# Kernel tuning notes

Hardware: AMD Instinct MI355X
Metric: run time of the kernel (lower is better)

Reference implementation:

```python
import jax, jax.numpy as jnp
import numpy as np

N_NODES = 50000
N_EDGES = 400000
F_IN = 70
E_DIM = 4
HID = 128
HEADS = 4


def _add_self_loops(src, dst, edge_attr, n):
    # PyG GATConv(add_self_loops=True, fill_value='mean' when edge_dim is set):
    # self-loop edge_attr = per-dst-node mean of incoming edge_attr.
    cnt = jax.ops.segment_sum(jnp.ones((src.shape[0],), edge_attr.dtype), dst, n)
    loop_attr = jax.ops.segment_sum(edge_attr, dst, n) / jnp.clip(cnt, 1.0)[:, None]
    loop = jnp.arange(n, dtype=src.dtype)
    return (jnp.concatenate([src, loop]), jnp.concatenate([dst, loop]),
            jnp.concatenate([edge_attr, loop_attr], axis=0))


def _gat_layer(x, src, dst, e_attr, W, a_src, a_dst, We, a_edge, b, concat):
    # W: [in, H*D]; a_src/a_dst/a_edge: [H, D]; We: [edge_dim, H*D]
    n = x.shape[0]
    H, D = a_src.shape
    xs = (x @ W).reshape(n, H, D)                      # [N,H,D]
    s_src = jnp.einsum('nhd,hd->nh', xs, a_src)        # [N,H]
    s_dst = jnp.einsum('nhd,hd->nh', xs, a_dst)
    ee = (e_attr @ We).reshape(-1, H, D)               # [E,H,D]
    s_edge = jnp.einsum('ehd,hd->eh', ee, a_edge)
    alpha = jax.nn.leaky_relu(s_src[src] + s_dst[dst] + s_edge, 0.2)  # [E,H]
    # segment softmax over edges grouped by destination node
    m = jax.ops.segment_max(alpha, dst, n)
    m = jnp.where(jnp.isfinite(m), m, 0.0)
    ex = jnp.exp(alpha - m[dst])
    denom = jax.ops.segment_sum(ex, dst, n)
    alpha = ex / (denom[dst] + 1e-16)
    msg = xs[src] * alpha[..., None]                   # [E,H,D] -- dominant traffic
    agg = jax.ops.segment_sum(msg, dst, n)             # [N,H,D]
    out = agg.reshape(n, H * D) if concat else agg.mean(axis=1)
    return out + b


def _layer_norm(x, g, b, eps=1e-5):
    mu = x.mean(-1, keepdims=True)
    var = ((x - mu) ** 2).mean(-1, keepdims=True)
    return (x - mu) * jax.lax.rsqrt(var + eps) * g + b


def setup_inputs() -> dict:
    key = jax.random.key(0)
    ks = jax.random.split(key, 24)
    f32 = jnp.float32
    node_features = jax.random.normal(ks[0], (N_NODES, F_IN), f32)
    edge_index = jax.random.randint(ks[1], (2, N_EDGES), 0, N_NODES, jnp.int32)
    edge_attr = jax.random.uniform(ks[2], (N_EDGES, E_DIM), f32)
    s = 0.1
    return {
        'node_features': node_features,
        'edge_index': edge_index,
        'edge_attr': edge_attr,
        'W1': jax.random.normal(ks[3], (F_IN, HEADS * HID), f32) * s,
        'as1': jax.random.normal(ks[4], (HEADS, HID), f32) * s,
        'ad1': jax.random.normal(ks[5], (HEADS, HID), f32) * s,
        'We1': jax.random.normal(ks[6], (E_DIM, HEADS * HID), f32) * s,
        'ae1': jax.random.normal(ks[7], (HEADS, HID), f32) * s,
        'b1': jnp.zeros((HEADS * HID,), f32),
        # GAT layer 2: 512 -> 128, 1 head, mean
        'W2': jax.random.normal(ks[8], (HEADS * HID, HID), f32) * s,
        'as2': jax.random.normal(ks[9], (1, HID), f32) * s,
        'ad2': jax.random.normal(ks[10], (1, HID), f32) * s,
        'We2': jax.random.normal(ks[11], (E_DIM, HID), f32) * s,
        'ae2': jax.random.normal(ks[12], (1, HID), f32) * s,
        'b2': jnp.zeros((HID,), f32),
        'ln_g': jnp.ones((HID,), f32),
        'ln_b': jnp.zeros((HID,), f32),
        'pw': jax.random.normal(ks[13], (HID, 8), f32) * s,
        'pb': jnp.zeros((8,), f32),
        'dw': jax.random.normal(ks[14], (HID, 4), f32) * s,
        'db': jnp.zeros((4,), f32),
    }


def reference(node_features, edge_index, edge_attr, W1, as1, ad1, We1, ae1, b1,
              W2, as2, ad2, We2, ae2, b2, ln_g, ln_b, pw, pb, dw, db):
    n = node_features.shape[0]
    src, dst, ea = _add_self_loops(edge_index[0], edge_index[1], edge_attr, n)
    x = jax.nn.gelu(_gat_layer(node_features, src, dst, ea, W1, as1, ad1, We1, ae1, b1, True), approximate=False)
    x = jax.nn.gelu(_gat_layer(x, src, dst, ea, W2, as2, ad2, We2, ae2, b2, False), approximate=False)
    x = _layer_norm(x, ln_g, ln_b)
    return (x @ pw + pb, x @ dw + db)
```

## Files before the change

kernel.cpp:

```cpp
#include <hip/hip_runtime.h>
#include <hip/hip_bf16.h>
#include <math.h>

#define NN 50000
#define NE 400000
#define FIN 70
#define EDIM 4
#define HIDD 128
#define NHEAD 4
constexpr int ET = NE + NN;
constexpr int KP1 = 96;
constexpr int NFP = 72;
constexpr int SCB = (NN + 255) / 256;

constexpr size_t al4(size_t x){ return (x + 3) & ~size_t(3); }
constexpr size_t CNT_O   = 0;
constexpr size_t ZEND    = al4(CNT_O + NN);
constexpr size_t CSR_O   = ZEND;
constexpr size_t BSUM_O  = al4(CSR_O + NN + 1);
constexpr size_t BOFF_O  = al4(BSUM_O + 256);
constexpr size_t EPK_O   = al4(BOFF_O + 256);
constexpr size_t EXF1_O  = al4(EPK_O + (size_t)ET*4);
constexpr size_t EXF2_O  = al4(EXF1_O + (size_t)ET*4);
constexpr size_t SS1_O   = al4(EXF2_O + ET);
constexpr size_t SD1_O   = al4(SS1_O + (size_t)NN*4);
constexpr size_t SS2_O   = al4(SD1_O + (size_t)NN*4);
constexpr size_t SD2_O   = al4(SS2_O + NN);
constexpr size_t CST_O   = al4(SD2_O + NN);
constexpr size_t W1T_O   = al4(CST_O + 2048);
constexpr size_t W2T_O   = al4(W1T_O + 4*128*KP1/2);
constexpr size_t NFB_O   = al4(W2T_O + 128*512/2);
constexpr size_t AGG_O   = al4(NFB_O + (size_t)NN*NFP/2);
constexpr size_t XS2_O   = al4(AGG_O + (size_t)4*NN*KP1/2);

constexpr int VS1 = 0;
constexpr int VD1 = 320;
constexpr int VE1 = 640;
constexpr int VE2 = 656;
constexpr int VS2 = 704;
constexpr int VD2 = 1216;

typedef short s8v __attribute__((ext_vector_type(8)));
typedef float f4v __attribute__((ext_vector_type(4)));

__device__ __forceinline__ unsigned short f2b(float v){
  __hip_bfloat16 b = __float2bfloat16(v);
  return *(unsigned short*)&b;
}
__device__ __forceinline__ float b2f(unsigned u_lo16){
  return __uint_as_float(u_lo16 << 16);
}
__device__ __forceinline__ unsigned pk2(float lo, float hi){
  return (unsigned)f2b(lo) | ((unsigned)f2b(hi) << 16);
}
__device__ __forceinline__ float lrelu(float x){ return x > 0.f ? x : 0.2f * x; }

__device__ __forceinline__ float gelu_fast(float x){
  float z = x * 0.70710678118654752440f;
  float a = fabsf(z);
  float t = 1.f / (1.f + 0.3275911f * a);
  float p = ((((1.061405429f*t - 1.453152027f)*t + 1.421413741f)*t
              - 0.284496736f)*t + 0.254829592f)*t;
  float erfv = 1.f - p * __expf(-a * a);
  erfv = copysignf(erfv, z);
  return 0.5f * x * (1.f + erfv);
}

__global__ void k_deg(const int* __restrict__ ei, int* __restrict__ cnt){
  int e = blockIdx.x * 256 + threadIdx.x;
  if (e >= NE) return;
  atomicAdd(&cnt[ei[NE + e]], 1);
}

__global__ void k_scan1(const int* __restrict__ cnt, int* __restrict__ bsum){
  __shared__ int ws[4];
  int t = threadIdx.x, lane = t & 63, w = t >> 6;
  int i = blockIdx.x * 256 + t;
  int v = (i < NN) ? cnt[i] + 1 : 0;
  for (int o = 32; o; o >>= 1) v += __shfl_down(v, o);
  if (lane == 0) ws[w] = v;
  __syncthreads();
  if (t == 0) bsum[blockIdx.x] = ws[0] + ws[1] + ws[2] + ws[3];
}

__global__ void k_scan2(const int* __restrict__ bsum, int* __restrict__ boff){
  __shared__ int ws[4];
  int t = threadIdx.x, lane = t & 63, w = t >> 6;
  int v = (t < SCB) ? bsum[t] : 0;
  int x = v;
  #pragma unroll
  for (int o = 1; o < 64; o <<= 1){ int u = __shfl_up(x, o); if (lane >= o) x += u; }
  if (lane == 63) ws[w] = x;
  __syncthreads();
  if (w == 0 && lane < 4){
    int y = ws[lane];
    #pragma unroll
    for (int o = 1; o < 4; o <<= 1){ int u = __shfl_up(y, o); if (lane >= o) y += u; }
    ws[lane] = y;
  }
  __syncthreads();
  int incl = x + (w > 0 ? ws[w - 1] : 0);
  if (t < SCB) boff[t] = incl - v;
}

__global__ void k_scan3(const int* __restrict__ cnt, const int* __restrict__ boff,
                        int* __restrict__ csr){
  __shared__ int ws[4];
  int t = threadIdx.x, lane = t & 63, w = t >> 6;
  int i = blockIdx.x * 256 + t;
  int v = (i < NN) ? cnt[i] + 1 : 0;
  int x = v;
  #pragma unroll
  for (int o = 1; o < 64; o <<= 1){ int u = __shfl_up(x, o); if (lane >= o) x += u; }
  if (lane == 63) ws[w] = x;
  __syncthreads();
  if (w == 0 && lane < 4){
    int y = ws[lane];
    #pragma unroll
    for (int o = 1; o < 4; o <<= 1){ int u = __shfl_up(y, o); if (lane >= o) y += u; }
    ws[lane] = y;
  }
  __syncthreads();
  if (i < NN) csr[i + 1] = boff[blockIdx.x] + (w > 0 ? ws[w - 1] : 0) + x;
  if (i == 0) csr[0] = 0;
}

__global__ void k_fill(const int* __restrict__ ei, const float* __restrict__ ea,
                       const int* __restrict__ csr, int* __restrict__ cnt,
                       int4* __restrict__ epk, const float* __restrict__ ss1,
                       const float* __restrict__ sd1, const float* __restrict__ C,
                       float4* __restrict__ exf){
  int e = blockIdx.x * 256 + threadIdx.x;
  if (e >= NE) return;
  int s = ei[e], d = ei[NE + e];
  int r = atomicSub(&cnt[d], 1);
  int p = csr[d] + r - 1;
  float4 a = *(const float4*)&ea[(size_t)e * 4];
  epk[p] = make_int4(s, d, (int)pk2(a.x, a.y), (int)pk2(a.z, a.w));
  float4 ssv = *(const float4*)&ss1[(size_t)s * 4];
  float4 sdv = *(const float4*)&sd1[(size_t)d * 4];
  float e0 = __expf(lrelu(ssv.x + sdv.x + a.x*C[VE1+0] + a.y*C[VE1+4] + a.z*C[VE1+8]  + a.w*C[VE1+12]));
  float e1 = __expf(lrelu(ssv.y + sdv.y + a.x*C[VE1+1] + a.y*C[VE1+5] + a.z*C[VE1+9]  + a.w*C[VE1+13]));
  float e2 = __expf(lrelu(ssv.z + sdv.z + a.x*C[VE1+2] + a.y*C[VE1+6] + a.z*C[VE1+10] + a.w*C[VE1+14]));
  float e3 = __expf(lrelu(ssv.w + sdv.w + a.x*C[VE1+3] + a.y*C[VE1+7] + a.z*C[VE1+11] + a.w*C[VE1+15]));
  exf[p] = make_float4(e0, e1, e2, e3);
}

__global__ void k_loopself(const int* __restrict__ csr, int4* __restrict__ epk,
                           const float* __restrict__ ss1, const float* __restrict__ sd1,
                           const float* __restrict__ C, float4* __restrict__ exf){
  int n = blockIdx.x * 256 + threadIdx.x;
  if (n >= NN) return;
  int a = csr[n], b = csr[n + 1];
  int deg = b - a - 1;
  float s0 = 0.f, s1 = 0.f, s2 = 0.f, s3 = 0.f;
  for (int p = a; p < b - 1; ++p){
    int4 v = epk[p];
    s0 += b2f((unsigned)v.z & 0xffffu); s1 += b2f((unsigned)v.z >> 16);
    s2 += b2f((unsigned)v.w & 0xffffu); s3 += b2f((unsigned)v.w >> 16);
  }
  float inv = 1.f / (float)(deg > 1 ? deg : 1);
  float m0 = s0*inv, m1 = s1*inv, m2 = s2*inv, m3 = s3*inv;
  epk[b - 1] = make_int4(n, n, (int)pk2(m0, m1), (int)pk2(m2, m3));
  float4 ssv = *(const float4*)&ss1[(size_t)n * 4];
  float4 sdv = *(const float4*)&sd1[(size_t)n * 4];
  float e0 = __expf(lrelu(ssv.x + sdv.x + m0*C[VE1+0] + m1*C[VE1+4] + m2*C[VE1+8]  + m3*C[VE1+12]));
  float e1 = __expf(lrelu(ssv.y + sdv.y + m0*C[VE1+1] + m1*C[VE1+5] + m2*C[VE1+9]  + m3*C[VE1+13]));
  float e2 = __expf(lrelu(ssv.z + sdv.z + m0*C[VE1+2] + m1*C[VE1+6] + m2*C[VE1+10] + m3*C[VE1+14]));
  float e3 = __expf(lrelu(ssv.w + sdv.w + m0*C[VE1+3] + m1*C[VE1+7] + m2*C[VE1+11] + m3*C[VE1+15]));
  exf[b - 1] = make_float4(e0, e1, e2, e3);
}

__global__ void k_prep(const float* __restrict__ W1, const float* __restrict__ as1,
                       const float* __restrict__ ad1, const float* __restrict__ We1,
                       const float* __restrict__ ae1, const float* __restrict__ W2,
                       const float* __restrict__ as2, const float* __restrict__ ad2,
                       const float* __restrict__ We2, const float* __restrict__ ae2,
                       float* __restrict__ C){
  int t = threadIdx.x;
  if (t < 280){
    int k = t >> 2, h = t & 3;
    float s = 0.f, d = 0.f;
    for (int dd = 0; dd < 128; ++dd){
      float w = W1[k*512 + h*128 + dd];
      s += w * as1[h*128 + dd];
      d += w * ad1[h*128 + dd];
    }
    C[VS1 + t] = s; C[VD1 + t] = d;
  }
  if (t < 16){
    int k = t >> 2, h = t & 3;
    float s = 0.f;
    for (int dd = 0; dd < 128; ++dd) s += We1[k*512 + h*128 + dd] * ae1[h*128 + dd];
    C[VE1 + t] = s;
  }
  if (t < 4){
    float s = 0.f;
    for (int dd = 0; dd < 128; ++dd) s += We2[t*128 + dd] * ae2[dd];
    C[VE2 + t] = s;
  }
  {
    float s = 0.f, d = 0.f;
    for (int dd = 0; dd < 128; ++dd){
      float w = W2[t*128 + dd];
      s += w * as2[dd];
      d += w * ad2[dd];
    }
    C[VS2 + t] = s; C[VD2 + t] = d;
  }
}

__global__ void k_tw(const float* __restrict__ W1, const float* __restrict__ W2,
                     unsigned short* __restrict__ W1t, unsigned short* __restrict__ W2t){
  int i = blockIdx.x * 256 + threadIdx.x;
  if (i < 4*128*KP1){
    int k = i % KP1, n = (i / KP1) & 127, h = i / (KP1*128);
    float v = (k < FIN) ? W1[k*512 + h*128 + n] : 0.f;
    W1t[i] = f2b(v);
  } else {
    int j = i - 4*128*KP1;
    if (j < 128*512){
      int k = j & 511, n = j >> 9;
      W2t[j] = f2b(W2[k*128 + n]);
    }
  }
}

__global__ __launch_bounds__(256) void k_cnfs1(const float* __restrict__ nf,
    const float* __restrict__ C, unsigned short* __restrict__ nfb,
    float* __restrict__ ss1, float* __restrict__ sd1){
  int lane = threadIdx.x & 63, w = threadIdx.x >> 6;
  int n = blockIdx.x * 4 + w;
  if (n >= NN) return;
  int c0 = lane * 2;
  bool act = lane < 35;
  float v0 = 0.f, v1 = 0.f;
  if (act){
    v0 = nf[(size_t)n * FIN + c0];
    v1 = nf[(size_t)n * FIN + c0 + 1];
  }
  if (lane < 36) *(unsigned*)&nfb[(size_t)n * NFP + c0] = act ? pk2(v0, v1) : 0u;
  float sh[4] = {0,0,0,0}, dh[4] = {0,0,0,0};
  if (act){
    float4 cs0 = *(const float4*)&C[VS1 + c0*4];
    float4 cs1 = *(const float4*)&C[VS1 + (c0+1)*4];
    float4 cd0 = *(const float4*)&C[VD1 + c0*4];
    float4 cd1 = *(const float4*)&C[VD1 + (c0+1)*4];
    sh[0] = v0*cs0.x + v1*cs1.x; sh[1] = v0*cs0.y + v1*cs1.y;
    sh[2] = v0*cs0.z + v1*cs1.z; sh[3] = v0*cs0.w + v1*cs1.w;
    dh[0] = v0*cd0.x + v1*cd1.x; dh[1] = v0*cd0.y + v1*cd1.y;
    dh[2] = v0*cd0.z + v1*cd1.z; dh[3] = v0*cd0.w + v1*cd1.w;
  }
  #pragma unroll
  for (int o = 32; o; o >>= 1){
    #pragma unroll
    for (int h = 0; h < 4; ++h){
      sh[h] += __shfl_xor(sh[h], o);
      dh[h] += __shfl_xor(dh[h], o);
    }
  }
  if (lane == 0){
    *(float4*)&ss1[(size_t)n*4] = make_float4(sh[0], sh[1], sh[2], sh[3]);
    *(float4*)&sd1[(size_t)n*4] = make_float4(dh[0], dh[1], dh[2], dh[3]);
  }
}

__global__ void k_al2(const int4* __restrict__ epk, const float* __restrict__ ss2,
                      const float* __restrict__ sd2, const float* __restrict__ C,
                      float* __restrict__ ex2){
  int p = blockIdx.x * 256 + threadIdx.x;
  if (p >= ET) return;
  int4 pk = epk[p];
  int s = pk.x, d = pk.y;
  float ax = b2f((unsigned)pk.z & 0xffffu), ay = b2f((unsigned)pk.z >> 16);
  float az = b2f((unsigned)pk.w & 0xffffu), aw = b2f((unsigned)pk.w >> 16);
  ex2[p] = __expf(lrelu(ss2[s] + sd2[d] +
             ax*C[VE2] + ay*C[VE2+1] + az*C[VE2+2] + aw*C[VE2+3]));
}

__global__ __launch_bounds__(256) void k_gemm12(
    const unsigned short* __restrict__ agg, const unsigned short* __restrict__ W1t,
    const unsigned short* __restrict__ W2t, const float* __restrict__ b1,
    const float* __restrict__ Cv, unsigned short* __restrict__ xs2b,
    float* __restrict__ ss2, float* __restrict__ sd2){
  __shared__ unsigned short xt[32 * 520];
  __shared__ unsigned short Bs[128 * 40];
  __shared__ unsigned short As[32 * 40];
  __shared__ float ssp[32][2], sdp[32][2];
  int tid = threadIdx.x, lane = tid & 63, w = tid >> 6;
  int wm = w & 1, wn = w >> 1;
  int m15 = lane & 15, rq = lane >> 4;
  int r0 = blockIdx.x * 32;
  int lrow = wm * 16 + m15;
  float s2a = 0.f, s2d = 0.f;
  constexpr size_t HS = (size_t)NN * KP1;
  for (int h = 0; h < 4; ++h){
    f4v acc[4] = {};
    const unsigned short* Ah = agg + (size_t)h * HS;
    const unsigned short* Wh = W1t + h * 128 * KP1;
    for (int k0 = 0; k0 < KP1; k0 += 32){
      if (tid < 128){
        int r = tid >> 2, c = tid & 3;
        int gr = r0 + r; if (gr >= NN) gr = NN - 1;
        *(uint4*)&As[r*40 + c*8] = *(const uint4*)&Ah[(size_t)gr*KP1 + k0 + c*8];
      }
      #pragma unroll
      for (int i = 0; i < 2; ++i){
        int idx = tid + i*256;
        int r = idx >> 2, c = idx & 3;
        *(uint4*)&Bs[r*40 + c*8] = *(const uint4*)&Wh[r*KP1 + k0 + c*8];
      }
      __syncthreads();
      s8v af = *(const s8v*)&As[lrow*40 + rq*8];
      #pragma unroll
      for (int ni = 0; ni < 4; ++ni){
        s8v bf = *(const s8v*)&Bs[(wn*64 + ni*16 + m15)*40 + rq*8];
        acc[ni] = __builtin_amdgcn_mfma_f32_16x16x32_bf16(bf, af, acc[ni], 0, 0, 0);
      }
      __syncthreads();
    }
    #pragma unroll
    for (int ni = 0; ni < 4; ++ni){
      int cb = h*128 + wn*64 + ni*16 + rq*4;
      float4 bv = *(const float4*)&b1[cb];
      float v0 = gelu_fast(acc[ni][0] + bv.x);
      float v1 = gelu_fast(acc[ni][1] + bv.y);
      float v2 = gelu_fast(acc[ni][2] + bv.z);
      float v3 = gelu_fast(acc[ni][3] + bv.w);
      float4 cs = *(const float4*)&Cv[VS2 + cb];
      float4 cd = *(const float4*)&Cv[VD2 + cb];
      s2a += v0*cs.x + v1*cs.y + v2*cs.z + v3*cs.w;
      s2d += v0*cd.x + v1*cd.y + v2*cd.z + v3*cd.w;
      *(uint2*)&xt[lrow*520 + cb] = make_uint2(pk2(v0,v1), pk2(v2,v3));
    }
  }
  s2a += __shfl_xor(s2a, 16); s2a += __shfl_xor(s2a, 32);
  s2d += __shfl_xor(s2d, 16); s2d += __shfl_xor(s2d, 32);
  if (rq == 0){ ssp[lrow][wn] = s2a; sdp[lrow][wn] = s2d; }
  __syncthreads();
  if (tid < 32 && r0 + tid < NN){
    ss2[r0 + tid] = ssp[tid][0] + ssp[tid][1];
    sd2[r0 + tid] = sdp[tid][0] + sdp[tid][1];
  }
  f4v acc2[4] = {};
  for (int k0 = 0; k0 < 512; k0 += 32){
    #pragma unroll
    for (int i = 0; i < 2; ++i){
      int idx = tid + i*256;
      int r = idx >> 2, c = idx & 3;
      *(uint4*)&Bs[r*40 + c*8] = *(const uint4*)&W2t[r*512 + k0 + c*8];
    }
    __syncthreads();
    s8v af = *(const s8v*)&xt[lrow*520 + k0 + rq*8];
    #pragma unroll
    for (int ni = 0; ni < 4; ++ni){
      s8v bf = *(const s8v*)&Bs[(wn*64 + ni*16 + m15)*40 + rq*8];
      acc2[ni] = __builtin_amdgcn_mfma_f32_16x16x32_bf16(bf, af, acc2[ni], 0, 0, 0);
    }
    __syncthreads();
  }
  int grow = r0 + lrow;
  if (grow < NN){
    #pragma unroll
    for (int ni = 0; ni < 4; ++ni){
      int gc = wn*64 + ni*16 + rq*4;
      *(uint2*)&xs2b[(size_t)grow*128 + gc] =
          make_uint2(pk2(acc2[ni][0], acc2[ni][1]), pk2(acc2[ni][2], acc2[ni][3]));
    }
  }
}

__global__ __launch_bounds__(256) void k_aggnf(const int* __restrict__ csr,
    const int4* __restrict__ epk, const float4* __restrict__ exf,
    const unsigned short* __restrict__ nfb, unsigned short* __restrict__ agg){
  int lane = threadIdx.x & 63, w = threadIdx.x >> 6;
  int n = blockIdx.x * 4 + w;
  if (n >= NN) return;
  int off = __builtin_amdgcn_readfirstlane(csr[n]);
  int end = __builtin_amdgcn_readfirstlane(csr[n + 1]);
  int col = lane * 2;
  bool act = lane < 36;
  float d0=0,d1=0,d2=0,d3=0;
  float a00=0,a01=0,a10=0,a11=0,a20=0,a21=0,a30=0,a31=0;
  int p = off;
  for (; p + 2 <= end; p += 2){
    int s0 = epk[p].x, s1 = epk[p+1].x;
    float4 e0 = exf[p], e1 = exf[p+1];
    unsigned u0 = 0, u1 = 0;
    if (act){
      u0 = *(const unsigned*)&nfb[(size_t)s0 * NFP + col];
      u1 = *(const unsigned*)&nfb[(size_t)s1 * NFP + col];
    }
    d0 += e0.x + e1.x; d1 += e0.y + e1.y; d2 += e0.z + e1.z; d3 += e0.w + e1.w;
    float v00 = b2f(u0 & 0xffffu), v01 = b2f(u0 >> 16);
    float v10 = b2f(u1 & 0xffffu), v11 = b2f(u1 >> 16);
    a00 += e0.x*v00 + e1.x*v10; a01 += e0.x*v01 + e1.x*v11;
    a10 += e0.y*v00 + e1.y*v10; a11 += e0.y*v01 + e1.y*v11;
    a20 += e0.z*v00 + e1.z*v10; a21 += e0.z*v01 + e1.z*v11;
    a30 += e0.w*v00 + e1.w*v10; a31 += e0.w*v01 + e1.w*v11;
  }
  if (p < end){
    int s0 = epk[p].x;
    float4 e0 = exf[p];
    unsigned u0 = 0;
    if (act) u0 = *(const unsigned*)&nfb[(size_t)s0 * NFP + col];
    d0 += e0.x; d1 += e0.y; d2 += e0.z; d3 += e0.w;
    float v00 = b2f(u0 & 0xffffu), v01 = b2f(u0 >> 16);
    a00 += e0.x*v00; a01 += e0.x*v01;
    a10 += e0.y*v00; a11 += e0.y*v01;
    a20 += e0.z*v00; a21 += e0.z*v01;
    a30 += e0.w*v00; a31 += e0.w*v01;
  }
  float i0 = 1.f/(d0+1e-16f), i1 = 1.f/(d1+1e-16f);
  float i2 = 1.f/(d2+1e-16f), i3 = 1.f/(d3+1e-16f);
  constexpr size_t HS = (size_t)NN * KP1;
  size_t base = (size_t)n * KP1 + col;
  if (act){
    *(unsigned*)&agg[base]        = pk2(a00*i0, a01*i0);
    *(unsigned*)&agg[base +   HS] = pk2(a10*i1, a11*i1);
    *(unsigned*)&agg[base + 2*HS] = pk2(a20*i2, a21*i2);
    *(unsigned*)&agg[base + 3*HS] = pk2(a30*i3, a31*i3);
  } else if (lane < 48){
    *(unsigned*)&agg[base]        = 0u;
    *(unsigned*)&agg[base +   HS] = 0u;
    *(unsigned*)&agg[base + 2*HS] = 0u;
    *(unsigned*)&agg[base + 3*HS] = 0u;
  }
}

__global__ __launch_bounds__(256) void k_agg2(
    const int* __restrict__ csr, const int4* __restrict__ epk,
    const float* __restrict__ ex2, const unsigned short* __restrict__ xs2b,
    const float* __restrict__ b2, const float* __restrict__ lng,
    const float* __restrict__ lnb, const float* __restrict__ pw,
    const float* __restrict__ pb, const float* __restrict__ dwm,
    const float* __restrict__ dbv, float* __restrict__ out){
  int lane = threadIdx.x & 63, w = threadIdx.x >> 6;
  int n = blockIdx.x * 4 + w;
  if (n >= NN) return;
  int off = __builtin_amdgcn_readfirstlane(csr[n]);
  int end = __builtin_amdgcn_readfirstlane(csr[n + 1]);
  int c0 = lane * 2;
  float acc0 = 0.f, acc1 = 0.f, den = 0.f;
  int p = off;
  for (; p + 4 <= end; p += 4){
    int s0 = epk[p].x, s1 = epk[p+1].x, s2 = epk[p+2].x, s3 = epk[p+3].x;
    float e0 = ex2[p], e1 = ex2[p+1], e2 = ex2[p+2], e3 = ex2[p+3];
    unsigned u0 = *(const unsigned*)&xs2b[(size_t)s0 * 128 + c0];
    unsigned u1 = *(const unsigned*)&xs2b[(size_t)s1 * 128 + c0];
    unsigned u2 = *(const unsigned*)&xs2b[(size_t)s2 * 128 + c0];
    unsigned u3 = *(const unsigned*)&xs2b[(size_t)s3 * 128 + c0];
    den += (e0 + e1) + (e2 + e3);
    acc0 += e0*b2f(u0 & 0xffffu) + e1*b2f(u1 & 0xffffu)
          + e2*b2f(u2 & 0xffffu) + e3*b2f(u3 & 0xffffu);
    acc1 += e0*b2f(u0 >> 16) + e1*b2f(u1 >> 16)
          + e2*b2f(u2 >> 16) + e3*b2f(u3 >> 16);
  }
  for (; p + 2 <= end; p += 2){
    int s0 = epk[p].x, s1 = epk[p+1].x;
    float e0 = ex2[p], e1 = ex2[p+1];
    unsigned u0 = *(const unsigned*)&xs2b[(size_t)s0 * 128 + c0];
    unsigned u1 = *(const unsigned*)&xs2b[(size_t)s1 * 128 + c0];
    den += e0 + e1;
    acc0 += e0*b2f(u0 & 0xffffu) + e1*b2f(u1 & 0xffffu);
    acc1 += e0*b2f(u0 >> 16) + e1*b2f(u1 >> 16);
  }
  if (p < end){
    int s0 = epk[p].x;
    float e0 = ex2[p];
    unsigned u0 = *(const unsigned*)&xs2b[(size_t)s0 * 128 + c0];
    den += e0;
    acc0 += e0*b2f(u0 & 0xffffu);
    acc1 += e0*b2f(u0 >> 16);
  }
  float invd = 1.f / (den + 1e-16f);
  float g0 = gelu_fast(acc0 * invd + b2[c0]);
  float g1 = gelu_fast(acc1 * invd + b2[c0 + 1]);
  float s = g0 + g1;
  #pragma unroll
  for (int o = 32; o; o >>= 1) s += __shfl_xor(s, o);
  float mu = s * (1.f / 128.f);
  float e0 = g0 - mu, e1 = g1 - mu;
  float q = e0*e0 + e1*e1;
  #pragma unroll
  for (int o = 32; o; o >>= 1) q += __shfl_xor(q, o);
  float rstd = rsqrtf(q * (1.f / 128.f) + 1e-5f);
  float y0 = e0 * rstd * lng[c0] + lnb[c0];
  float y1 = e1 * rstd * lng[c0 + 1] + lnb[c0 + 1];
  float pr[12];
  #pragma unroll
  for (int jj = 0; jj < 8; ++jj) pr[jj] = y0 * pw[c0*8 + jj] + y1 * pw[(c0+1)*8 + jj];
  #pragma unroll
  for (int jj = 0; jj < 4; ++jj) pr[8+jj] = y0 * dwm[c0*4 + jj] + y1 * dwm[(c0+1)*4 + jj];
  #pragma unroll
  for (int o = 32; o; o >>= 1)
    #pragma unroll
    for (int jj = 0; jj < 12; ++jj) pr[jj] += __shfl_xor(pr[jj], o);
  if (lane == 0){
    #pragma unroll
    for (int jj = 0; jj < 8; ++jj) out[(size_t)n*8 + jj] = pr[jj] + pb[jj];
    #pragma unroll
    for (int jj = 0; jj < 4; ++jj) out[(size_t)NN*8 + (size_t)n*4 + jj] = pr[8+jj] + dbv[jj];
  }
}

extern "C" void kernel_launch(void* const* d_in, const int* in_sizes, int n_in,
                              void* d_out, int out_size, void* d_ws, size_t ws_size,
                              hipStream_t stream){
  const float* nf  = (const float*)d_in[0];
  const int*   ei  = (const int*)  d_in[1];
  const float* ea  = (const float*)d_in[2];
  const float* W1  = (const float*)d_in[3];
  const float* as1 = (const float*)d_in[4];
  const float* ad1 = (const float*)d_in[5];
  const float* We1 = (const float*)d_in[6];
  const float* ae1 = (const float*)d_in[7];
  const float* b1  = (const float*)d_in[8];
  const float* W2  = (const float*)d_in[9];
  const float* as2 = (const float*)d_in[10];
  const float* ad2 = (const float*)d_in[11];
  const float* We2 = (const float*)d_in[12];
  const float* ae2 = (const float*)d_in[13];
  const float* b2  = (const float*)d_in[14];
  const float* lng = (const float*)d_in[15];
  const float* lnb = (const float*)d_in[16];
  const float* pw  = (const float*)d_in[17];
  const float* pb  = (const float*)d_in[18];
  const float* dw  = (const float*)d_in[19];
  const float* db  = (const float*)d_in[20];
  float* out = (float*)d_out;

  float* wf = (float*)d_ws;
  int*      cnt  = (int*)     (wf + CNT_O);
  int*      csr  = (int*)     (wf + CSR_O);
  int*      bsum = (int*)     (wf + BSUM_O);
  int*      boff = (int*)     (wf + BOFF_O);
  int4*     epk  = (int4*)    (wf + EPK_O);
  float4*   exf1 = (float4*)  (wf + EXF1_O);
  float*    ex2  =            (wf + EXF2_O);
  float*    ss1  =            (wf + SS1_O);
  float*    sd1  =            (wf + SD1_O);
  float*    ss2  =            (wf + SS2_O);
  float*    sd2  =            (wf + SD2_O);
  float*    Cc   =            (wf + CST_O);
  unsigned short* W1t = (unsigned short*)(wf + W1T_O);
  unsigned short* W2t = (unsigned short*)(wf + W2T_O);
  unsigned short* nfb = (unsigned short*)(wf + NFB_O);
  unsigned short* agg = (unsigned short*)(wf + AGG_O);
  unsigned short* xs2b= (unsigned short*)(wf + XS2_O);

  hipMemsetAsync(cnt, 0, NN * sizeof(int), stream);
  k_prep<<<1, 512, 0, stream>>>(W1, as1, ad1, We1, ae1, W2, as2, ad2, We2, ae2, Cc);
  k_tw<<<(4*128*KP1 + 128*512 + 255) / 256, 256, 0, stream>>>(W1, W2, W1t, W2t);
  k_cnfs1<<<(NN + 3) / 4, 256, 0, stream>>>(nf, Cc, nfb, ss1, sd1);
  k_deg<<<(NE + 255) / 256, 256, 0, stream>>>(ei, cnt);
  k_scan1<<<SCB, 256, 0, stream>>>(cnt, bsum);
  k_scan2<<<1, 256, 0, stream>>>(bsum, boff);
  k_scan3<<<SCB, 256, 0, stream>>>(cnt, boff, csr);
  k_fill<<<(NE + 255) / 256, 256, 0, stream>>>(ei, ea, csr, cnt, epk, ss1, sd1, Cc, exf1);
  k_loopself<<<(NN + 255) / 256, 256, 0, stream>>>(csr, epk, ss1, sd1, Cc, exf1);
  k_aggnf<<<(NN + 3) / 4, 256, 0, stream>>>(csr, epk, exf1, nfb, agg);
  k_gemm12<<<(NN + 31) / 32, 256, 0, stream>>>(agg, W1t, W2t, b1, Cc, xs2b, ss2, sd2);
  k_al2<<<(ET + 255) / 256, 256, 0, stream>>>(epk, ss2, sd2, Cc, ex2);
  k_agg2<<<(NN + 3) / 4, 256, 0, stream>>>(csr, epk, ex2, xs2b,
                                           b2, lng, lnb, pw, pb, dw, db, out);
}
```

Baseline: 364.2 us.

## Double-buffer and register-prefetch B tiles in fused GEMM kernel, load A directly

Restructures k_gemm12 so the weight tiles are prefetched into registers one step ahead and written into a double-buffered shared-memory array, removing one __syncthreads per k-step. The A operand (aggregated features) is now read straight from global memory into MFMA fragments, prefetched one head ahead, instead of being staged through shared memory. Shared padding changes from 40/520 to 36/516 and launch bounds request three blocks per CU. The aim is to overlap global loads with MFMA work and cut barrier stalls, at the cost of more registers and possible LDS bank conflicts from the new padding.

```diff
diff --git a/kernel.cpp b/kernel.cpp
--- a/kernel.cpp
+++ b/kernel.cpp
@@ -278,93 +278,124 @@
              ax*C[VE2] + ay*C[VE2+1] + az*C[VE2+2] + aw*C[VE2+3]));
 }
 
-__global__ __launch_bounds__(256) void k_gemm12(
+__global__ __launch_bounds__(256, 3) void k_gemm12(
     const unsigned short* __restrict__ agg, const unsigned short* __restrict__ W1t,
     const unsigned short* __restrict__ W2t, const float* __restrict__ b1,
     const float* __restrict__ Cv, unsigned short* __restrict__ xs2b,
     float* __restrict__ ss2, float* __restrict__ sd2){
-  __shared__ unsigned short xt[32 * 520];
-  __shared__ unsigned short Bs[128 * 40];
-  __shared__ unsigned short As[32 * 40];
+  __shared__ unsigned short xt[32 * 516];
+  __shared__ unsigned short Bs[2][128 * 36];
   __shared__ float ssp[32][2], sdp[32][2];
   int tid = threadIdx.x, lane = tid & 63, w = tid >> 6;
   int wm = w & 1, wn = w >> 1;
   int m15 = lane & 15, rq = lane >> 4;
   int r0 = blockIdx.x * 32;
   int lrow = wm * 16 + m15;
+  int gr = r0 + lrow; if (gr >= NN) gr = NN - 1;
   float s2a = 0.f, s2d = 0.f;
   constexpr size_t HS = (size_t)NN * KP1;
+
+  int br0 = tid >> 2, bc0 = tid & 3;
+  int br1 = br0 + 64;
+  int bw0 = br0 * 36 + bc0 * 8;
+  int bw1 = br1 * 36 + bc0 * 8;
+
+  uint4 breg0 = *(const uint4*)&W1t[br0 * KP1 + bc0 * 8];
+  uint4 breg1 = *(const uint4*)&W1t[br1 * KP1 + bc0 * 8];
+  s8v afc0, afc1, afc2, afn0, afn1, afn2;
+  {
+    const unsigned short* Ah = agg + (size_t)gr * KP1 + rq * 8;
+    afc0 = *(const s8v*)(Ah);
+    afc1 = *(const s8v*)(Ah + 32);
+    afc2 = *(const s8v*)(Ah + 64);
+  }
+
   for (int h = 0; h < 4; ++h){
     f4v acc[4] = {};
-    const unsigned short* Ah = agg + (size_t)h * HS;
-    const unsigned short* Wh = W1t + h * 128 * KP1;
-    for (int k0 = 0; k0 < KP1; k0 += 32){
-      if (tid < 128){
-        int r = tid >> 2, c = tid & 3;
-        int gr = r0 + r; if (gr >= NN) gr = NN - 1;
-        *(uint4*)&As[r*40 + c*8] = *(const uint4*)&Ah[(size_t)gr*KP1 + k0 + c*8];
+    #pragma unroll
+    for (int kf = 0; kf < 3; ++kf){
+      int buf = (h * 3 + kf) & 1;
+      unsigned short* Bb = Bs[buf];
+      *(uint4*)&Bb[bw0] = breg0;
+      *(uint4*)&Bb[bw1] = breg1;
+      __syncthreads();
+      if (kf == 0 && h < 3){
+        const unsigned short* Ah = agg + (size_t)(h + 1) * HS + (size_t)gr * KP1 + rq * 8;
+        afn0 = *(const s8v*)(Ah);
+        afn1 = *(const s8v*)(Ah + 32);
+        afn2 = *(const s8v*)(Ah + 64);
       }
-      #pragma unroll
-      for (int i = 0; i < 2; ++i){
-        int idx = tid + i*256;
-        int r = idx >> 2, c = idx & 3;
-        *(uint4*)&Bs[r*40 + c*8] = *(const uint4*)&Wh[r*KP1 + k0 + c*8];
+      if (kf < 2){
+        const unsigned short* Wn = W1t + h * (128 * KP1) + (kf + 1) * 32;
+        breg0 = *(const uint4*)&Wn[br0 * KP1 + bc0 * 8];
+        breg1 = *(const uint4*)&Wn[br1 * KP1 + bc0 * 8];
+      } else if (h < 3){
+        const unsigned short* Wn = W1t + (h + 1) * (128 * KP1);
+        breg0 = *(const uint4*)&Wn[br0 * KP1 + bc0 * 8];
+        breg1 = *(const uint4*)&Wn[br1 * KP1 + bc0 * 8];
+      } else {
+        breg0 = *(const uint4*)&W2t[br0 * 512 + bc0 * 8];
+        breg1 = *(const uint4*)&W2t[br1 * 512 + bc0 * 8];
       }
-      __syncthreads();
-      s8v af = *(const s8v*)&As[lrow*40 + rq*8];
+      s8v af = (kf == 0) ? afc0 : (kf == 1) ? afc1 : afc2;
       #pragma unroll
       for (int ni = 0; ni < 4; ++ni){
-        s8v bf = *(const s8v*)&Bs[(wn*64 + ni*16 + m15)*40 + rq*8];
+        s8v bf = *(const s8v*)&Bb[(wn * 64 + ni * 16 + m15) * 36 + rq * 8];
         acc[ni] = __builtin_amdgcn_mfma_f32_16x16x32_bf16(bf, af, acc[ni], 0, 0, 0);
       }
-      __syncthreads();
-    }
-    #pragma unroll
-    for (int ni = 0; ni < 4; ++ni){
-      int cb = h*128 + wn*64 + ni*16 + rq*4;
-      float4 bv = *(const float4*)&b1[cb];
-      float v0 = gelu_fast(acc[ni][0] + bv.x);
-      float v1 = gelu_fast(acc[ni][1] + bv.y);
-      float v2 = gelu_fast(acc[ni][2] + bv.z);
-      float v3 = gelu_fast(acc[ni][3] + bv.w);
-      float4 cs = *(const float4*)&Cv[VS2 + cb];
-      float4 cd = *(const float4*)&Cv[VD2 + cb];
-      s2a += v0*cs.x + v1*cs.y + v2*cs.z + v3*cs.w;
-      s2d += v0*cd.x + v1*cd.y + v2*cd.z + v3*cd.w;
-      *(uint2*)&xt[lrow*520 + cb] = make_uint2(pk2(v0,v1), pk2(v2,v3));
+      if (kf == 2){
+        #pragma unroll
+        for (int ni = 0; ni < 4; ++ni){
+          int cb = h * 128 + wn * 64 + ni * 16 + rq * 4;
+          float4 bv = *(const float4*)&b1[cb];
+          float v0 = gelu_fast(acc[ni][0] + bv.x);
+          float v1 = gelu_fast(acc[ni][1] + bv.y);
+          float v2 = gelu_fast(acc[ni][2] + bv.z);
+          float v3 = gelu_fast(acc[ni][3] + bv.w);
+          float4 cs = *(const float4*)&Cv[VS2 + cb];
+          float4 cd = *(const float4*)&Cv[VD2 + cb];
+          s2a += v0*cs.x + v1*cs.y + v2*cs.z + v3*cs.w;
+          s2d += v0*cd.x + v1*cd.y + v2*cd.z + v3*cd.w;
+          *(uint2*)&xt[lrow * 516 + cb] = make_uint2(pk2(v0, v1), pk2(v2, v3));
+        }
+        afc0 = afn0; afc1 = afn1; afc2 = afn2;
+      }
     }
   }
   s2a += __shfl_xor(s2a, 16); s2a += __shfl_xor(s2a, 32);
   s2d += __shfl_xor(s2d, 16); s2d += __shfl_xor(s2d, 32);
   if (rq == 0){ ssp[lrow][wn] = s2a; sdp[lrow][wn] = s2d; }
-  __syncthreads();
-  if (tid < 32 && r0 + tid < NN){
-    ss2[r0 + tid] = ssp[tid][0] + ssp[tid][1];
-    sd2[r0 + tid] = sdp[tid][0] + sdp[tid][1];
-  }
+
   f4v acc2[4] = {};
-  for (int k0 = 0; k0 < 512; k0 += 32){
-    #pragma unroll
-    for (int i = 0; i < 2; ++i){
-      int idx = tid + i*256;
-      int r = idx >> 2, c = idx & 3;
-      *(uint4*)&Bs[r*40 + c*8] = *(const uint4*)&W2t[r*512 + k0 + c*8];
-    }
+  #pragma unroll 2
+  for (int p = 0; p < 16; ++p){
+    int buf = p & 1;
+    unsigned short* Bb = Bs[buf];
+    *(uint4*)&Bb[bw0] = breg0;
+    *(uint4*)&Bb[bw1] = breg1;
     __syncthreads();
-    s8v af = *(const s8v*)&xt[lrow*520 + k0 + rq*8];
+    if (p == 0 && tid < 32 && r0 + tid < NN){
+      ss2[r0 + tid] = ssp[tid][0] + ssp[tid][1];
+      sd2[r0 + tid] = sdp[tid][0] + sdp[tid][1];
+    }
+    if (p < 15){
+      const unsigned short* Wn = W2t + (p + 1) * 32;
+      breg0 = *(const uint4*)&Wn[br0 * 512 + bc0 * 8];
+      breg1 = *(const uint4*)&Wn[br1 * 512 + bc0 * 8];
+    }
+    s8v af = *(const s8v*)&xt[lrow * 516 + p * 32 + rq * 8];
     #pragma unroll
     for (int ni = 0; ni < 4; ++ni){
-      s8v bf = *(const s8v*)&Bs[(wn*64 + ni*16 + m15)*40 + rq*8];
+      s8v bf = *(const s8v*)&Bb[(wn * 64 + ni * 16 + m15) * 36 + rq * 8];
       acc2[ni] = __builtin_amdgcn_mfma_f32_16x16x32_bf16(bf, af, acc2[ni], 0, 0, 0);
     }
-    __syncthreads();
   }
   int grow = r0 + lrow;
   if (grow < NN){
     #pragma unroll
     for (int ni = 0; ni < 4; ++ni){
-      int gc = wn*64 + ni*16 + rq*4;
-      *(uint2*)&xs2b[(size_t)grow*128 + gc] =
+      int gc = wn * 64 + ni * 16 + rq * 4;
+      *(uint2*)&xs2b[(size_t)grow * 128 + gc] =
           make_uint2(pk2(acc2[ni][0], acc2[ni][1]), pk2(acc2[ni][2], acc2[ni][3]));
     }
   }
```

After: 436.1 us. +19.7%, slower.

## Prepack weights into MFMA fragment layout and load operands directly from global

Applied to the files above, without the earlier changes.

Rewrites the weight transpose kernel to emit W1 and W2 in a per-k-chunk fragment-major layout, so each lane of k_gemm12 can load its MFMA B operand straight from global/L2. The shared-memory staging buffers and all the per-k-step __syncthreads in both GEMM phases are removed, and the A operand for layer 1 is also read directly from global. The xt row pitch changes to 516 and launch bounds request 4 blocks per CU to raise occupancy. This trades LDS staging and barriers for redundant global/L2 reads of the small weight matrices across waves.

```diff
diff --git a/kernel.cpp b/kernel.cpp
--- a/kernel.cpp
+++ b/kernel.cpp
@@ -211,17 +211,19 @@
 }
 
 __global__ void k_tw(const float* __restrict__ W1, const float* __restrict__ W2,
-                     unsigned short* __restrict__ W1t, unsigned short* __restrict__ W2t){
+                     unsigned short* __restrict__ W1p, unsigned short* __restrict__ W2p){
   int i = blockIdx.x * 256 + threadIdx.x;
-  if (i < 4*128*KP1){
-    int k = i % KP1, n = (i / KP1) & 127, h = i / (KP1*128);
-    float v = (k < FIN) ? W1[k*512 + h*128 + n] : 0.f;
-    W1t[i] = f2b(v);
+  if (i < 12*128*32){
+    int kk = i & 31, r = (i >> 5) & 127, ph = i >> 12;
+    int h = ph / 3, kf = ph - 3*h;
+    int kg = kf*32 + kk;
+    float v = (kg < FIN) ? W1[kg*512 + h*128 + r] : 0.f;
+    W1p[i] = f2b(v);
   } else {
-    int j = i - 4*128*KP1;
-    if (j < 128*512){
-      int k = j & 511, n = j >> 9;
-      W2t[j] = f2b(W2[k*128 + n]);
+    int j = i - 12*128*32;
+    if (j < 16*128*32){
+      int kk = j & 31, r = (j >> 5) & 127, p = j >> 12;
+      W2p[j] = f2b(W2[(p*32 + kk)*128 + r]);
     }
   }
 }
@@ -278,50 +280,39 @@
              ax*C[VE2] + ay*C[VE2+1] + az*C[VE2+2] + aw*C[VE2+3]));
 }
 
-__global__ __launch_bounds__(256) void k_gemm12(
-    const unsigned short* __restrict__ agg, const unsigned short* __restrict__ W1t,
-    const unsigned short* __restrict__ W2t, const float* __restrict__ b1,
+__global__ __launch_bounds__(256, 4) void k_gemm12(
+    const unsigned short* __restrict__ agg, const unsigned short* __restrict__ W1p,
+    const unsigned short* __restrict__ W2p, const float* __restrict__ b1,
     const float* __restrict__ Cv, unsigned short* __restrict__ xs2b,
     float* __restrict__ ss2, float* __restrict__ sd2){
-  __shared__ unsigned short xt[32 * 520];
-  __shared__ unsigned short Bs[128 * 40];
-  __shared__ unsigned short As[32 * 40];
+  __shared__ unsigned short xt[32 * 516];
   __shared__ float ssp[32][2], sdp[32][2];
   int tid = threadIdx.x, lane = tid & 63, w = tid >> 6;
   int wm = w & 1, wn = w >> 1;
   int m15 = lane & 15, rq = lane >> 4;
   int r0 = blockIdx.x * 32;
   int lrow = wm * 16 + m15;
+  int gr = r0 + lrow; if (gr >= NN) gr = NN - 1;
   float s2a = 0.f, s2d = 0.f;
   constexpr size_t HS = (size_t)NN * KP1;
+  const int bfo = (wn * 64 + m15) * 32 + rq * 8;
+
   for (int h = 0; h < 4; ++h){
     f4v acc[4] = {};
-    const unsigned short* Ah = agg + (size_t)h * HS;
-    const unsigned short* Wh = W1t + h * 128 * KP1;
-    for (int k0 = 0; k0 < KP1; k0 += 32){
-      if (tid < 128){
-        int r = tid >> 2, c = tid & 3;
-        int gr = r0 + r; if (gr >= NN) gr = NN - 1;
-        *(uint4*)&As[r*40 + c*8] = *(const uint4*)&Ah[(size_t)gr*KP1 + k0 + c*8];
-      }
-      #pragma unroll
-      for (int i = 0; i < 2; ++i){
-        int idx = tid + i*256;
-        int r = idx >> 2, c = idx & 3;
-        *(uint4*)&Bs[r*40 + c*8] = *(const uint4*)&Wh[r*KP1 + k0 + c*8];
-      }
-      __syncthreads();
-      s8v af = *(const s8v*)&As[lrow*40 + rq*8];
+    const unsigned short* Ah = agg + (size_t)h * HS + (size_t)gr * KP1 + rq * 8;
+    #pragma unroll
+    for (int kf = 0; kf < 3; ++kf){
+      s8v af = *(const s8v*)(Ah + kf * 32);
+      const unsigned short* Bp = W1p + (h * 3 + kf) * 4096 + bfo;
       #pragma unroll
       for (int ni = 0; ni < 4; ++ni){
-        s8v bf = *(const s8v*)&Bs[(wn*64 + ni*16 + m15)*40 + rq*8];
+        s8v bf = *(const s8v*)(Bp + ni * 512);
         acc[ni] = __builtin_amdgcn_mfma_f32_16x16x32_bf16(bf, af, acc[ni], 0, 0, 0);
       }
-      __syncthreads();
     }
     #pragma unroll
     for (int ni = 0; ni < 4; ++ni){
-      int cb = h*128 + wn*64 + ni*16 + rq*4;
+      int cb = h * 128 + wn * 64 + ni * 16 + rq * 4;
       float4 bv = *(const float4*)&b1[cb];
       float v0 = gelu_fast(acc[ni][0] + bv.x);
       float v1 = gelu_fast(acc[ni][1] + bv.y);
@@ -331,40 +322,37 @@
       float4 cd = *(const float4*)&Cv[VD2 + cb];
       s2a += v0*cs.x + v1*cs.y + v2*cs.z + v3*cs.w;
       s2d += v0*cd.x + v1*cd.y + v2*cd.z + v3*cd.w;
-      *(uint2*)&xt[lrow*520 + cb] = make_uint2(pk2(v0,v1), pk2(v2,v3));
+      *(uint2*)&xt[lrow * 516 + cb] = make_uint2(pk2(v0, v1), pk2(v2, v3));
     }
   }
   s2a += __shfl_xor(s2a, 16); s2a += __shfl_xor(s2a, 32);
   s2d += __shfl_xor(s2d, 16); s2d += __shfl_xor(s2d, 32);
   if (rq == 0){ ssp[lrow][wn] = s2a; sdp[lrow][wn] = s2d; }
+
   __syncthreads();
+
   if (tid < 32 && r0 + tid < NN){
     ss2[r0 + tid] = ssp[tid][0] + ssp[tid][1];
     sd2[r0 + tid] = sdp[tid][0] + sdp[tid][1];
   }
+
   f4v acc2[4] = {};
-  for (int k0 = 0; k0 < 512; k0 += 32){
-    #pragma unroll
-    for (int i = 0; i < 2; ++i){
-      int idx = tid + i*256;
-      int r = idx >> 2, c = idx & 3;
-      *(uint4*)&Bs[r*40 + c*8] = *(const uint4*)&W2t[r*512 + k0 + c*8];
-    }
-    __syncthreads();
-    s8v af = *(const s8v*)&xt[lrow*520 + k0 + rq*8];
+  #pragma unroll 4
+  for (int p = 0; p < 16; ++p){
+    s8v af = *(const s8v*)&xt[lrow * 516 + p * 32 + rq * 8];
+    const unsigned short* Bp = W2p + p * 4096 + bfo;
     #pragma unroll
     for (int ni = 0; ni < 4; ++ni){
-      s8v bf = *(const s8v*)&Bs[(wn*64 + ni*16 + m15)*40 + rq*8];
+      s8v bf = *(const s8v*)(Bp + ni * 512);
       acc2[ni] = __builtin_amdgcn_mfma_f32_16x16x32_bf16(bf, af, acc2[ni], 0, 0, 0);
     }
-    __syncthreads();
   }
   int grow = r0 + lrow;
   if (grow < NN){
     #pragma unroll
     for (int ni = 0; ni < 4; ++ni){
-      int gc = wn*64 + ni*16 + rq*4;
-      *(uint2*)&xs2b[(size_t)grow*128 + gc] =
+      int gc = wn * 64 + ni * 16 + rq * 4;
+      *(uint2*)&xs2b[(size_t)grow * 128 + gc] =
           make_uint2(pk2(acc2[ni][0], acc2[ni][1]), pk2(acc2[ni][2], acc2[ni][3]));
     }
   }
@@ -543,15 +531,15 @@
   float*    ss2  =            (wf + SS2_O);
   float*    sd2  =            (wf + SD2_O);
   float*    Cc   =            (wf + CST_O);
-  unsigned short* W1t = (unsigned short*)(wf + W1T_O);
-  unsigned short* W2t = (unsigned short*)(wf + W2T_O);
+  unsigned short* W1p = (unsigned short*)(wf + W1T_O);
+  unsigned short* W2p = (unsigned short*)(wf + W2T_O);
   unsigned short* nfb = (unsigned short*)(wf + NFB_O);
   unsigned short* agg = (unsigned short*)(wf + AGG_O);
   unsigned short* xs2b= (unsigned short*)(wf + XS2_O);
 
   hipMemsetAsync(cnt, 0, NN * sizeof(int), stream);
   k_prep<<<1, 512, 0, stream>>>(W1, as1, ad1, We1, ae1, W2, as2, ad2, We2, ae2, Cc);
-  k_tw<<<(4*128*KP1 + 128*512 + 255) / 256, 256, 0, stream>>>(W1, W2, W1t, W2t);
+  k_tw<<<(12*128*32 + 16*128*32 + 255) / 256, 256, 0, stream>>>(W1, W2, W1p, W2p);
   k_cnfs1<<<(NN + 3) / 4, 256, 0, stream>>>(nf, Cc, nfb, ss1, sd1);
   k_deg<<<(NE + 255) / 256, 256, 0, stream>>>(ei, cnt);
   k_scan1<<<SCB, 256, 0, stream>>>(cnt, bsum);
@@ -560,7 +548,7 @@
   k_fill<<<(NE + 255) / 256, 256, 0, stream>>>(ei, ea, csr, cnt, epk, ss1, sd1, Cc, exf1);
   k_loopself<<<(NN + 255) / 256, 256, 0, stream>>>(csr, epk, ss1, sd1, Cc, exf1);
   k_aggnf<<<(NN + 3) / 4, 256, 0, stream>>>(csr, epk, exf1, nfb, agg);
-  k_gemm12<<<(NN + 31) / 32, 256, 0, stream>>>(agg, W1t, W2t, b1, Cc, xs2b, ss2, sd2);
+  k_gemm12<<<(NN + 31) / 32, 256, 0, stream>>>(agg, W1p, W2p, b1, Cc, xs2b, ss2, sd2);
   k_al2<<<(ET + 255) / 256, 256, 0, stream>>>(epk, ss2, sd2, Cc, ex2);
   k_agg2<<<(NN + 3) / 4, 256, 0, stream>>>(csr, epk, ex2, xs2b,
                                            b2, lng, lnb, pw, pb, dw, db, out);
```

After: 373.6 us. 2.6% more time.
